# Kernel tuning notes

Measured on AMD Instinct MI355X. Metric: run time of the kernel, lower is better.

The kernel has to match this reference:

```python
import jax, jax.numpy as jnp
import numpy as np

B, S, DIM = 1, 2048, 2048
HEADS, KV_HEADS = 32, 8
DH = DIM // HEADS          # 64 head dim
G = HEADS // KV_HEADS      # 4 grouped queries per kv head
CBLK = 16                  # compress block size (stride == block size)
SBLK = 16                  # selection (fine) block size
NSEL = 8                   # top-k selected blocks
WIN = 64                   # sliding window size
SCALE = DH ** -0.5
NEG = -1e30
CDIM = CBLK * DH


def setup_inputs():
    key = jax.random.key(0)
    ks = jax.random.split(key, 16)
    def rnd(i, shape, sc=0.02):
        return jax.random.normal(ks[i], shape, dtype=jnp.float32) * sc
    dim_inner, dim_kv = HEADS * DH, KV_HEADS * DH
    return {
        "hidden_states": jax.random.normal(ks[0], (B, S, DIM), dtype=jnp.float32),
        "w_qkv": rnd(1, (DIM, dim_inner + 2 * dim_kv)),
        "k_pos": rnd(2, (KV_HEADS, CBLK, DH)),
        "v_pos": rnd(3, (KV_HEADS, CBLK, DH)),
        "k_cw1": rnd(4, (CDIM, CDIM)), "k_cb1": jnp.zeros((CDIM,), jnp.float32),
        "k_cw2": rnd(5, (CDIM, DH)),  "k_cb2": jnp.zeros((DH,), jnp.float32),
        "v_cw1": rnd(6, (CDIM, CDIM)), "v_cb1": jnp.zeros((CDIM,), jnp.float32),
        "v_cw2": rnd(7, (CDIM, DH)),  "v_cb2": jnp.zeros((DH,), jnp.float32),
        "mem_ck": rnd(8, (KV_HEADS, 1, DH)),
        "mem_cv": rnd(9, (KV_HEADS, 1, DH)),
        "w_gate": rnd(10, (DIM, 3 * HEADS)),
        "b_gate": jnp.tile(jnp.array([-2.0, -2.0, 2.0], jnp.float32), HEADS),
        "w_out": rnd(11, (dim_inner, DIM)),
    }


def _rope(x, pos):
    # rotary-embedding-torch style: interleaved pairs (x0,x1),(x2,x3),...
    d = x.shape[-1]
    inv = 1.0 / (10000.0 ** (jnp.arange(0, d, 2, dtype=jnp.float32) / d))
    ang = pos[:, None] * inv[None, :]
    cos, sin = jnp.cos(ang), jnp.sin(ang)
    x1, x2 = x[..., 0::2], x[..., 1::2]
    return jnp.stack([x1 * cos - x2 * sin, x1 * sin + x2 * cos], axis=-1).reshape(x.shape)


def _forward(x, w_qkv, k_pos, v_pos, k_cw1, k_cb1, k_cw2, k_cb2,
             v_cw1, v_cb1, v_cw2, v_cb2, mem_ck, mem_cv, w_gate, b_gate, w_out):
    b, n, _ = x.shape
    di, dkv = HEADS * DH, KV_HEADS * DH
    qkv = x @ w_qkv
    # head index = kv_head * G + grouped_query, matching 'b n (h d) -> b h n d'
    q = qkv[..., :di].reshape(b, n, KV_HEADS, G, DH).transpose(0, 2, 3, 1, 4)    # [b,kh,g,n,d]
    k = qkv[..., di:di + dkv].reshape(b, n, KV_HEADS, DH).transpose(0, 2, 1, 3)  # [b,kh,n,d]
    v = qkv[..., di + dkv:].reshape(b, n, KV_HEADS, DH).transpose(0, 2, 1, 3)

    # ---- branch 1: compressed-block attention (pre-rotary q/k, intra-block abs pos) ----
    nc = n // CBLK
    kb = k[:, :, :nc * CBLK].reshape(b, KV_HEADS, nc, CBLK, DH) + k_pos[None, :, None]
    vb = v[:, :, :nc * CBLK].reshape(b, KV_HEADS, nc, CBLK, DH) + v_pos[None, :, None]
    ck = jax.nn.relu(kb.reshape(b, KV_HEADS, nc, CDIM) @ k_cw1 + k_cb1) @ k_cw2 + k_cb2
    cv = jax.nn.relu(vb.reshape(b, KV_HEADS, nc, CDIM) @ v_cw1 + v_cb1) @ v_cw2 + v_cb2
    ck = jnp.concatenate([jnp.broadcast_to(mem_ck[None], (b, KV_HEADS, 1, DH)), ck], axis=2)
    cv = jnp.concatenate([jnp.broadcast_to(mem_cv[None], (b, KV_HEADS, 1, DH)), cv], axis=2)
    csim = jnp.einsum('bhgnd,bhjd->bhgnj', q, ck) * SCALE
    ck_last = jnp.concatenate([jnp.array([-1]), (jnp.arange(nc) + 1) * CBLK - 1])
    cmask = ck_last[None, :] < jnp.arange(n)[:, None]                            # [n, 1+nc]
    csim = jnp.where(cmask, csim, NEG)
    c_out = jnp.einsum('bhgnj,bhjd->bhgnd', jax.nn.softmax(csim, -1), cv)

    # ---- importance scores -> top-k selected blocks (shared across grouped queries) ----
    imp = csim[..., 1:].mean(axis=2)                                             # [b,kh,n,nc]
    imp = jnp.concatenate([jnp.full(imp.shape[:-1] + (1,), -1e3, imp.dtype), imp], axis=-1)
    imp = jax.nn.softmax(imp, -1)[..., 1:]
    sel_vals, sel_idx = jax.lax.top_k(imp, NSEL)                                 # [b,kh,n,NSEL]
    fine_gate_mask = sel_vals > 1e-10

    # rotary for fine + sliding branches
    pos = jnp.arange(n, dtype=jnp.float32)
    rq, rk = _rope(q, pos), _rope(k, pos)

    # ---- branch 2: fine attention over top-k selected blocks + causal own block ----
    nf = n // SBLK
    own = jnp.broadcast_to((jnp.arange(n) // SBLK)[None, None, :, None], (b, KV_HEADS, n, 1))
    idx = jnp.concatenate([sel_idx, own], axis=-1)                               # [b,kh,n,NSEL+1]
    kblocks = rk.reshape(b, KV_HEADS, nf, SBLK, DH)
    vblocks = v.reshape(b, KV_HEADS, nf, SBLK, DH)
    bi = jnp.arange(b)[:, None, None, None]
    hi = jnp.arange(KV_HEADS)[None, :, None, None]
    fk = kblocks[bi, hi, idx].reshape(b, KV_HEADS, n, (NSEL + 1) * SBLK, DH)
    fv = vblocks[bi, hi, idx].reshape(b, KV_HEADS, n, (NSEL + 1) * SBLK, DH)
    sel_m = jnp.repeat(fine_gate_mask[..., None], SBLK, -1).reshape(b, KV_HEADS, n, NSEL * SBLK)
    diag_m = (jnp.arange(n) % SBLK)[:, None] >= jnp.arange(SBLK)[None, :]        # own-block causal
    fmask = jnp.concatenate(
        [sel_m, jnp.broadcast_to(diag_m[None, None], (b, KV_HEADS, n, SBLK))], axis=-1)
    fsim = jnp.einsum('bhgnd,bhnjd->bhgnj', rq, fk) * SCALE
    fsim = jnp.where(fmask[:, :, None], fsim, NEG)
    f_out = jnp.einsum('bhgnj,bhnjd->bhgnd', jax.nn.softmax(fsim, -1), fv)

    # ---- branch 3: sliding-window attention (current + previous window, exact size) ----
    nwin = n // WIN
    qw = rq.reshape(b, KV_HEADS, G, nwin, WIN, DH)
    kw = rk.reshape(b, KV_HEADS, nwin, WIN, DH)
    vw = v.reshape(b, KV_HEADS, nwin, WIN, DH)
    kcat = jnp.concatenate([jnp.concatenate([jnp.zeros_like(kw[:, :, :1]), kw[:, :, :-1]], 2), kw], 3)
    vcat = jnp.concatenate([jnp.concatenate([jnp.zeros_like(vw[:, :, :1]), vw[:, :, :-1]], 2), vw], 3)
    ssim = jnp.einsum('bhgwid,bhwjd->bhgwij', qw, kcat) * SCALE
    i_, j_ = jnp.arange(WIN), jnp.arange(2 * WIN)
    delta = i_[:, None] - (j_[None, :] - WIN)                                    # query - key distance
    smask = ((delta >= 0) & (delta <= WIN))[None] \
        & ((jnp.arange(nwin) > 0)[:, None, None] | (j_ >= WIN)[None, None, :])
    ssim = jnp.where(smask[None, None, None], ssim, NEG)
    s_out = jnp.einsum('bhgwij,bhwjd->bhgwid', jax.nn.softmax(ssim, -1), vcat)
    s_out = s_out.reshape(b, KV_HEADS, G, n, DH)

    # ---- learned sigmoid gate combine (compressed, fine, sliding) + out proj ----
    gates = jax.nn.sigmoid(x @ w_gate + b_gate).reshape(b, n, KV_HEADS, G, 3).transpose(0, 2, 3, 1, 4)
    out = gates[..., 0:1] * c_out + gates[..., 1:2] * f_out + gates[..., 2:3] * s_out
    out = out.transpose(0, 3, 1, 2, 4).reshape(b, n, HEADS * DH)
    return out @ w_out


def reference(hidden_states, w_qkv, k_pos, v_pos, k_cw1, k_cb1, k_cw2, k_cb2,
              v_cw1, v_cb1, v_cw2, v_cb2, mem_ck, mem_cv, w_gate, b_gate, w_out):
    return _forward(hidden_states, w_qkv, k_pos, v_pos, k_cw1, k_cb1, k_cw2, k_cb2,
                    v_cw1, v_cb1, v_cw2, v_cb2, mem_ck, mem_cv, w_gate, b_gate, w_out)
```

## Files before the change

### kernel.cpp

```cpp
#include <hip/hip_runtime.h>
#include <hip/hip_bf16.h>
#include <math.h>

using bf16 = __hip_bfloat16;
typedef __attribute__((ext_vector_type(8))) short short8;
typedef __attribute__((ext_vector_type(4))) float f32x4;

#define SCALE 0.125f
#define NEGV  -1e30f
#define QS    3200

__device__ __forceinline__ float bf2f(bf16 x) { return __bfloat162float(x); }
__device__ __forceinline__ bf16  f2bf(float x) { return __float2bfloat16(x); }
__device__ __forceinline__ short f2bs(float x) {
  bf16 b = __float2bfloat16(x);
  return *reinterpret_cast<short*>(&b);
}
__device__ __forceinline__ float dot4(float4 a, float4 b) {
  return a.x * b.x + a.y * b.y + a.z * b.z + a.w * b.w;
}
__device__ __forceinline__ float sigm(float x) { return 1.0f / (1.0f + __expf(-x)); }

__device__ __forceinline__ void wavefence() {
  asm volatile("s_waitcnt lgkmcnt(0)" ::: "memory");
// ... 232 lines not shown
{
  int idx = blockIdx.x * 256 + threadIdx.x;
  if (idx >= 8 * 160 * 64) return;
  int h = idx / (160 * 64), r = (idx >> 6) % 160, d = idx & 63;
  if (r >= 129) { cvT[((size_t)h * 64 + d) * 160 + r] = f2bf(0.f); return; }
  float kv, vv;
  if (r == 0) {
    kv = bf2f(mem_ck[h * 64 + d]);
    vv = bf2f(mem_cv[h * 64 + d]);
  } else {
    kv = ckpre[((size_t)h * 128 + r - 1) * 64 + d] + bf2f(k_cb2[d]);
    vv = cvpre[((size_t)h * 128 + r - 1) * 64 + d] + bf2f(v_cb2[d]);
  }
  ck[((size_t)h * 129 + r) * 64 + d] = kv;
  cvT[((size_t)h * 64 + d) * 160 + r] = f2bf(vv);
}

__global__ __launch_bounds__(256, 4)
void compress_attn_kernel(const float* __restrict__ qkv, const float* __restrict__ ck,
                          const bf16* __restrict__ cvT,
                          float* __restrict__ outpre, int* __restrict__ sel)
{
  __shared__ __align__(16) char un[4][5632];
  const int tid = threadIdx.x, w = tid >> 6, lane = tid & 63;
  const int quad = lane >> 4, l16 = lane & 15;
  const int h = blockIdx.x >> 7;
  const int jv = blockIdx.x & 127;
  const int i0 = jv * 16 + w * 4;
  float* qs = (float*)un[w];
  bf16*  ps = (bf16*)un[w];

  #pragma unroll
  for (int m = 0; m < 16; m++)
    qs[m * 64 + lane] = qkv[(size_t)(i0 + (m >> 2)) * QS + (h * 4 + (m & 3)) * 64 + lane];
  wavefence();

  const float* kh = ck + (size_t)h * 129 * 64;
  const float4* k0 = (const float4*)(kh + lane * 64);
  const float4* k1 = (const float4*)(kh + (lane + 64) * 64);
  const bool two = (jv >= 64);

  float d0[4][4], d1[4][4];
  #pragma unroll
  for (int T = 0; T < 4; T++)
    #pragma unroll
    for (int g = 0; g < 4; g++) { d0[T][g] = 0.f; d1[T][g] = 0.f; }

  if (two) {
    #pragma unroll 4
    for (int t = 0; t < 16; t++) {
      float4 a = k0[t], b = k1[t];
      #pragma unroll
      for (int T = 0; T < 4; T++)
        #pragma unroll
        for (int g = 0; g < 4; g++) {
          float4 qv = *(const float4*)&qs[(T * 4 + g) * 64 + t * 4];
          d0[T][g] += dot4(qv, a);
          d1[T][g] += dot4(qv, b);
        }
    }
  } else {
    #pragma unroll 4
    for (int t = 0; t < 16; t++) {
      float4 a = k0[t];
      #pragma unroll
      for (int T = 0; T < 4; T++)
        #pragma unroll
        for (int g = 0; g < 4; g++) {
          float4 qv = *(const float4*)&qs[(T * 4 + g) * 64 + t * 4];
          d0[T][g] += dot4(qv, a);
        }
    }
  }
  wavefence();

  const bool v0 = (lane == 0) || (lane <= jv);
  const bool v1 = two && (lane + 64 <= jv);
  float imp0[4], imp1[4];
  #pragma unroll
  for (int T = 0; T < 4; T++) {
    #pragma unroll
    for (int g = 0; g < 4; g++) {
      d0[T][g] = v0 ? d0[T][g] * SCALE : NEGV;
      d1[T][g] = v1 ? d1[T][g] * SCALE : NEGV;
    }
    imp0[T] = (d0[T][0] + d0[T][1] + d0[T][2] + d0[T][3]) * 0.25f;
    imp1[T] = (d1[T][0] + d1[T][1] + d1[T][2] + d1[T][3]) * 0.25f;
  }

  float mx[4][4], sm[4][4];
  #pragma unroll
  for (int T = 0; T < 4; T++)
    #pragma unroll
    for (int g = 0; g < 4; g++) mx[T][g] = fmaxf(d0[T][g], d1[T][g]);
  #pragma unroll
  for (int off = 32; off; off >>= 1)
    #pragma unroll
    for (int T = 0; T < 4; T++)
      #pragma unroll
      for (int g = 0; g < 4; g++) mx[T][g] = fmaxf(mx[T][g], __shfl_xor(mx[T][g], off));
  #pragma unroll
  for (int T = 0; T < 4; T++)
    #pragma unroll
    for (int g = 0; g < 4; g++) {
      d0[T][g] = __expf(d0[T][g] - mx[T][g]);
      d1[T][g] = __expf(d1[T][g] - mx[T][g]);
      sm[T][g] = d0[T][g] + d1[T][g];
    }
  #pragma unroll
  for (int off = 32; off; off >>= 1)
    #pragma unroll
    for (int T = 0; T < 4; T++)
      #pragma unroll
      for (int g = 0; g < 4; g++) sm[T][g] += __shfl_xor(sm[T][g], off);
  #pragma unroll
  for (int T = 0; T < 4; T++)
    #pragma unroll
    for (int g = 0; g < 4; g++) {
      float inv = 1.0f / sm[T][g];
      ps[(T * 4 + g) * 176 + lane] = f2bf(d0[T][g] * inv);
      if (two) ps[(T * 4 + g) * 176 + 64 + lane] = f2bf(d1[T][g] * inv);
    }

  float q0[4], q1[4];
  {
    float mxi[4], smi[4], e0[4], e1[4];
    #pragma unroll
    for (int T = 0; T < 4; T++) {
      float iv0 = (lane == 0) ? -1000.0f : imp0[T];
      mxi[T] = fmaxf(iv0, imp1[T]);
      q0[T] = iv0;
      q1[T] = imp1[T];
    }
    #pragma unroll
    for (int off = 32; off; off >>= 1)
      #pragma unroll
      for (int T = 0; T < 4; T++) mxi[T] = fmaxf(mxi[T], __shfl_xor(mxi[T], off));
    #pragma unroll
    for (int T = 0; T < 4; T++) {
      e0[T] = __expf(q0[T] - mxi[T]);
      e1[T] = __expf(q1[T] - mxi[T]);
      smi[T] = e0[T] + e1[T];
    }
    #pragma unroll
    for (int off = 32; off; off >>= 1)
      #pragma unroll
      for (int T = 0; T < 4; T++) smi[T] += __shfl_xor(smi[T], off);
    #pragma unroll
    for (int T = 0; T < 4; T++) {
      float inv = 1.0f / smi[T];
      q0[T] = (lane >= 1) ? e0[T] * inv : -1.0f;
      q1[T] = e1[T] * inv;
    }
  }
  for (int s = 0; s < 8; s++) {
    float bv[4]; int bj[4];
    #pragma unroll
    for (int T = 0; T < 4; T++) {
      bv[T] = q0[T]; bj[T] = lane;
      if (q1[T] > bv[T]) { bv[T] = q1[T]; bj[T] = lane + 64; }
    }
    #pragma unroll
    for (int off = 32; off; off >>= 1)
      #pragma unroll
      for (int T = 0; T < 4; T++) {
        float ov = __shfl_xor(bv[T], off); int oj = __shfl_xor(bj[T], off);
        if (ov > bv[T] || (ov == bv[T] && oj < bj[T])) { bv[T] = ov; bj[T] = oj; }
      }
    #pragma unroll
    for (int T = 0; T < 4; T++) {
      if (lane == 0)
        sel[((size_t)h * 2048 + i0 + T) * 8 + s] = (bv[T] > 1e-10f) ? (bj[T] - 1) : -1;
      if (bj[T] == lane)           q0[T] = -1.0f;
      else if (bj[T] == lane + 64) q1[T] = -1.0f;
    }
  }

  const int iq = i0 + quad;
  float g0v[4];
  #pragma unroll
  for (int g = 0; g < 4; g++)
    g0v[g] = sigm(qkv[(size_t)iq * QS + 3072 + (h * 4 + g) * 3 + 0]);
  wavefence();

  const bf16* cvh = cvT + (size_t)h * 64 * 160;
  const int nks = (jv >> 5) + 1;
  f32x4 acc[4];
  #pragma unroll
  for (int dt = 0; dt < 4; dt++) acc[dt] = f32x4{0, 0, 0, 0};
  for (int ks = 0; ks < nks; ks++) {
    short8 ap = *(const short8*)(const void*)&ps[l16 * 176 + ks * 32 + quad * 8];
    #pragma unroll
    for (int dt = 0; dt < 4; dt++) {
      const bf16* cp = cvh + (size_t)(dt * 16 + l16) * 160 + ks * 32 + quad * 8;
      short8 bv = *(const short8*)(const void*)cp;
      acc[dt] = __builtin_amdgcn_mfma_f32_16x16x32_bf16(ap, bv, acc[dt], 0, 0, 0);
    }
  }

  #pragma unroll
  for (int g = 0; g < 4; g++) {
    const int hq = h * 4 + g;
    #pragma unroll
    for (int dt = 0; dt < 4; dt++)
      outpre[(size_t)iq * 2048 + hq * 64 + dt * 16 + l16] = g0v[g] * acc[dt][g];
  }
}

__global__ __launch_bounds__(256)
void rope_kernel(const float* __restrict__ qkv, bf16* __restrict__ qb,
                 bf16* __restrict__ kb)
{
  int idx = blockIdx.x * 256 + threadIdx.x;
  if (idx >= 2048 * 40 * 32) return;
  int m = idx & 31, hh = (idx >> 5) % 40, i = idx / 1280;
  int col = (hh < 32) ? hh * 64 + 2 * m : 2048 + (hh - 32) * 64 + 2 * m;
  const float* p = qkv + (size_t)i * QS + col;
  float x1 = p[0], x2 = p[1];
  float inv = exp2f(-0.41524101186092029f * (float)m);
  float ang = (float)i * inv;
  float s, c;
  __sincosf(ang, &s, &c);
  float r1 = x1 * c - x2 * s;
  float r2 = x1 * s + x2 * c;
  unsigned pack = ((unsigned)(unsigned short)f2bs(r1)) |
                  (((unsigned)(unsigned short)f2bs(r2)) << 16);
  if (hh < 32) {
    int h = hh >> 2, g = hh & 3;
    *(unsigned*)&qb[(((size_t)h * 2048 + i) * 4 + g) * 64 + 2 * m] = pack;
  } else {
    *(unsigned*)&kb[((size_t)(hh - 32) * 2048 + i) * 64 + 2 * m] = pack;
  }
}

__global__ __launch_bounds__(256)
void slide_attn_kernel(const float* __restrict__ qkv, const bf16* __restrict__ qb,
                       const bf16* __restrict__ kb, const bf16* __restrict__ vt,
                       bf16* __restrict__ oslide)
{
  __shared__ __align__(16) bf16 ps[4][16][104];
  const int tid = threadIdx.x, w = tid >> 6, lane = tid & 63;
  const int quad = lane >> 4, l16 = lane & 15;
  const int h = blockIdx.x >> 7, i0 = (blockIdx.x & 127) << 4;
  const int g = w;

  const bf16* qp = qb + (((size_t)h * 2048 + i0 + l16) * 4 + g) * 64 + quad * 8;
  short8 aq0 = *(const short8*)(const void*)qp;
  short8 aq1 = *(const short8*)(const void*)(qp + 32);

  const bf16* kbh = kb + (size_t)h * 2048 * 64;
  const int jbase = i0 - 64;

  f32x4 cs[5];
  #pragma unroll
  for (int t = 0; t < 5; t++) {
    int jr = jbase + t * 16 + l16;
    int jc = jr < 0 ? 0 : jr;
    const bf16* kp = kbh + (size_t)jc * 64 + quad * 8;
    short8 b0 = *(const short8*)(const void*)kp;
    short8 b1 = *(const short8*)(const void*)(kp + 32);
    f32x4 c = {0.f, 0.f, 0.f, 0.f};
    c = __builtin_amdgcn_mfma_f32_16x16x32_bf16(aq0, b0, c, 0, 0, 0);
    c = __builtin_amdgcn_mfma_f32_16x16x32_bf16(aq1, b1, c, 0, 0, 0);
    cs[t] = c;
  }

  float pr[5][4];
  #pragma unroll
  for (int r = 0; r < 4; r++) {
    int ti = i0 + quad * 4 + r;
    float mx = -3.0e38f;
    #pragma unroll
    for (int t = 0; t < 5; t++) {
      int j = jbase + t * 16 + l16;
      bool valid = (j >= 0) && (j >= ti - 64) && (j <= ti);
      float sv = valid ? cs[t][r] * SCALE : -3.0e38f;
      pr[t][r] = sv;
      mx = fmaxf(mx, sv);
    }
    #pragma unroll
    for (int off = 8; off; off >>= 1) mx = fmaxf(mx, __shfl_xor(mx, off));
    float sm = 0.f;
    #pragma unroll
    for (int t = 0; t < 5; t++) { float e = __expf(pr[t][r] - mx); pr[t][r] = e; sm += e; }
    #pragma unroll
    for (int off = 8; off; off >>= 1) sm += __shfl_xor(sm, off);
    float inv = 1.0f / sm;
    #pragma unroll
    for (int t = 0; t < 5; t++) pr[t][r] *= inv;
  }

  #pragma unroll
  for (int t = 0; t < 5; t++)
    #pragma unroll
    for (int r = 0; r < 4; r++)
      ps[w][quad * 4 + r][t * 16 + l16] = f2bf(pr[t][r]);
  #pragma unroll
  for (int r = 0; r < 4; r++) ps[w][l16][80 + quad * 4 + r] = f2bf(0.f);
  wavefence();

  const bf16* vth = vt + (size_t)h * 64 * 2176 + 64;
  f32x4 os[4];
  #pragma unroll
  for (int dt = 0; dt < 4; dt++) os[dt] = f32x4{0,0,0,0};
  #pragma unroll
  for (int ks = 0; ks < 3; ks++) {
    short8 ap = *(const short8*)(const void*)&ps[w][l16][ks * 32 + quad * 8];
    int coff = jbase + ks * 32 + quad * 8;
    #pragma unroll
    for (int dt = 0; dt < 4; dt++) {
      const bf16* vp = vth + (size_t)(dt * 16 + l16) * 2176 + coff;
      short8 bv = *(const short8*)(const void*)vp;
      os[dt] = __builtin_amdgcn_mfma_f32_16x16x32_bf16(ap, bv, os[dt], 0, 0, 0);
    }
  }

  #pragma unroll
  for (int r = 0; r < 4; r++) {
    int ti = i0 + quad * 4 + r;
    int hq = h * 4 + g;
    float g2 = sigm(qkv[(size_t)ti * QS + 3072 + hq * 3 + 2]);
    #pragma unroll
    for (int dt = 0; dt < 4; dt++)
      oslide[(size_t)ti * 2048 + hq * 64 + dt * 16 + l16] = f2bf(g2 * os[dt][r]);
  }
}

__global__ __launch_bounds__(256)
void fine_attn_kernel(const float* __restrict__ qkv, const int* __restrict__ sel,
                      const float* __restrict__ outpre, const bf16* __restrict__ oslide,
                      const bf16* __restrict__ qb, const bf16* __restrict__ kb,
                      const bf16* __restrict__ vt, bf16* __restrict__ outpre_b)
{
  __shared__ __align__(16) bf16 psf[4][16][176];
  const int tid = threadIdx.x, w = tid >> 6, lane = tid & 63;
  const int quad = lane >> 4, l16 = lane & 15;
  const int h = blockIdx.x >> 7;
  const int i0 = (blockIdx.x & 127) * 16 + w * 4;

  const bf16* qp = qb + (((size_t)h * 2048 + i0 + (l16 >> 2)) * 4 + (l16 & 3)) * 64 + quad * 8;
  short8 aq0 = *(const short8*)(const void*)qp;
  short8 aq1 = *(const short8*)(const void*)(qp + 32);

  const bf16* kbh = kb + (size_t)h * 2048 * 64;
  const int own = i0 >> 4;
  const int selbase = (h * 2048 + i0) * 8;

  f32x4 ct[9];

  {
    const bf16* kp = kbh + (size_t)(own * 16 + l16) * 64 + quad * 8;
    short8 b0 = *(const short8*)(const void*)kp;
    short8 b1 = *(const short8*)(const void*)(kp + 32);
    f32x4 c = {0.f, 0.f, 0.f, 0.f};
    c = __builtin_amdgcn_mfma_f32_16x16x32_bf16(aq0, b0, c, 0, 0, 0);
    c = __builtin_amdgcn_mfma_f32_16x16x32_bf16(aq1, b1, c, 0, 0, 0);
    const int imod = (i0 + quad) & 15;
    #pragma unroll
    for (int g = 0; g < 4; g++)
      ct[8][g] = (l16 <= imod) ? c[g] * SCALE : -3.0e38f;
  }

  int vb[4][8];
  #pragma unroll
  for (int T = 0; T < 4; T++) {
    #pragma unroll
    for (int t = 0; t < 8; t++) {
      int blk = __builtin_amdgcn_readfirstlane(sel[selbase + T * 8 + t]);
      bool tv = (blk >= 0);
      int blc = tv ? blk : 0;
      vb[T][t] = blc;
      const bf16* kp = kbh + (size_t)(blc * 16 + l16) * 64 + quad * 8;
      short8 b0 = *(const short8*)(const void*)kp;
      short8 b1 = *(const short8*)(const void*)(kp + 32);
      f32x4 c = {0.f, 0.f, 0.f, 0.f};
      c = __builtin_amdgcn_mfma_f32_16x16x32_bf16(aq0, b0, c, 0, 0, 0);
      c = __builtin_amdgcn_mfma_f32_16x16x32_bf16(aq1, b1, c, 0, 0, 0);
      #pragma unroll
      for (int g = 0; g < 4; g++) {
        float v = tv ? c[g] * SCALE : -3.0e38f;
        if (T == 0) ct[t][g] = v;
        else if (quad == T) ct[t][g] = v;
      }
    }
  }

  float fm[4], fsum[4];
  #pragma unroll
  for (int g = 0; g < 4; g++) fm[g] = -3.0e38f;
  #pragma unroll
  for (int t = 0; t < 9; t++)
    #pragma unroll
    for (int g = 0; g < 4; g++) fm[g] = fmaxf(fm[g], ct[t][g]);
  #pragma unroll
  for (int g = 0; g < 4; g++) {
    #pragma unroll
    for (int off = 8; off; off >>= 1) fm[g] = fmaxf(fm[g], __shfl_xor(fm[g], off));
    fsum[g] = 0.f;
  }
  #pragma unroll
  for (int t = 0; t < 9; t++)
    #pragma unroll
    for (int g = 0; g < 4; g++) {
      float e = __expf(ct[t][g] - fm[g]);
      ct[t][g] = e;
      fsum[g] += e;
    }
  #pragma unroll
  for (int g = 0; g < 4; g++) {
    #pragma unroll
    for (int off = 8; off; off >>= 1) fsum[g] += __shfl_xor(fsum[g], off);
    fsum[g] = 1.0f / fsum[g];
  }

  #pragma unroll
  for (int t = 0; t < 9; t++)
    #pragma unroll
    for (int g = 0; g < 4; g++)
      psf[w][quad * 4 + g][t * 16 + l16] = f2bf(ct[t][g] * fsum[g]);
  #pragma unroll
  for (int g = 0; g < 4; g++)
    psf[w][quad * 4 + g][144 + l16] = f2bf(0.f);

  const int iq = i0 + quad;
  float g1v[4], prev[4][4];
  #pragma unroll
  for (int g = 0; g < 4; g++) {
    const int hq = h * 4 + g;
    g1v[g] = sigm(qkv[(size_t)iq * QS + 3072 + hq * 3 + 1]);
    #pragma unroll
    for (int dt = 0; dt < 4; dt++) {
      size_t oidx = (size_t)iq * 2048 + hq * 64 + dt * 16 + l16;
      prev[g][dt] = outpre[oidx] + bf2f(oslide[oidx]);
    }
  }
  wavefence();

  const bf16* vth = vt + (size_t)h * 64 * 2176 + 64;

  f32x4 obase[4];
  {
    short8 ap = *(const short8*)(const void*)&psf[w][l16][128 + quad * 8];
    int coff = (((quad >> 1) == 0) ? own : 0) * 16 + (quad & 1) * 8;
    #pragma unroll
    for (int dt = 0; dt < 4; dt++) {
      const bf16* vp = vth + (size_t)(dt * 16 + l16) * 2176 + coff;
      short8 bv = *(const short8*)(const void*)vp;
      f32x4 z = {0.f, 0.f, 0.f, 0.f};
      obase[dt] = __builtin_amdgcn_mfma_f32_16x16x32_bf16(ap, bv, z, 0, 0, 0);
    }
  }

  f32x4 osave[4];
  #pragma unroll
  for (int T = 0; T < 4; T++) {
    f32x4 acc[4];
    #pragma unroll
    for (int dt = 0; dt < 4; dt++) acc[dt] = obase[dt];
    #pragma unroll
    for (int ks = 0; ks < 4; ks++) {
      short8 ap = *(const short8*)(const void*)&psf[w][l16][ks * 32 + quad * 8];
      int blkv = ((quad >> 1) == 0) ? vb[T][ks * 2] : vb[T][ks * 2 + 1];
      int coff = blkv * 16 + (quad & 1) * 8;
      #pragma unroll
      for (int dt = 0; dt < 4; dt++) {
        const bf16* vp = vth + (size_t)(dt * 16 + l16) * 2176 + coff;
        short8 bv = *(const short8*)(const void*)vp;
        acc[dt] = __builtin_amdgcn_mfma_f32_16x16x32_bf16(ap, bv, acc[dt], 0, 0, 0);
      }
    }
    #pragma unroll
    for (int dt = 0; dt < 4; dt++) {
      if (T == 0) osave[dt] = acc[dt];
      else if (quad == T) osave[dt] = acc[dt];
    }
  }

  #pragma unroll
  for (int g = 0; g < 4; g++) {
    const int hq = h * 4 + g;
    #pragma unroll
    for (int dt = 0; dt < 4; dt++) {
      size_t oidx = (size_t)iq * 2048 + hq * 64 + dt * 16 + l16;
      outpre_b[oidx] = f2bf(prev[g][dt] + g1v[g] * osave[dt][g]);
    }
  }
}

extern "C" void kernel_launch(void* const* d_in, const int* in_sizes, int n_in,
                              void* d_out, int out_size, void* d_ws, size_t ws_size,
                              hipStream_t stream)
{
  char* ws = (char*)d_ws;
  size_t off = 0;
  auto alloc = [&](size_t bytes) -> char* {
    char* p = ws + off; off = (off + bytes + 255) & ~(size_t)255; return p;
  };

  int* flag = (int*)alloc(256);
  bf16* inb[17];
  for (int i = 0; i < 17; i++) {
    if (i == 1 || i == 4 || i == 8 || i == 14 || i == 16) { inb[i] = nullptr; continue; }
    inb[i] = (bf16*)alloc((size_t)in_sizes[i] * sizeof(bf16));
  }
  bf16* w_qkvT = (bf16*)alloc(3200ull * 2048 * 2);
  bf16* k_cw1T = (bf16*)alloc(1024ull * 1024 * 2);
  bf16* v_cw1T = (bf16*)alloc(1024ull * 1024 * 2);
  bf16* w_outT = (bf16*)alloc(2048ull * 2048 * 2);

  float* qkv      = (float*)alloc(2048ull * QS * 4);
  float* outpre   = (float*)alloc(2048ull * 2048 * 4);
  bf16*  kvb      = (bf16*)alloc(2048ull * 1024 * 2);
  bf16*  hid      = (bf16*)alloc(2048ull * 1024 * 2);
  float* ckcvpre  = (float*)alloc(2048ull * 64 * 4);
  float* ckb      = (float*)alloc(8ull * 129 * 64 * 4);
  int*   sel      = (int*)alloc(8ull * 2048 * 8 * 4);
  bf16*  qbuf     = (bf16*)alloc(8ull * 2048 * 4 * 64 * 2);
  bf16*  kbuf     = (bf16*)alloc(8ull * 2048 * 64 * 2);
  bf16*  vtb      = (bf16*)alloc(8ull * 64 * 2176 * 2);
  bf16*  outpre_b = kvb;
  bf16*  cvT      = k_cw1T;
  bf16*  oslide   = (bf16*)w_qkvT;

  const bf16 *xb = inb[0], *k_posb = inb[2], *v_posb = inb[3],
             *k_cb1b = inb[5], *k_cw2b = inb[6], *k_cb2b = inb[7],
             *v_cb1b = inb[9], *v_cw2b = inb[10], *v_cb2b = inb[11],
             *mem_ckb = inb[12], *mem_cvb = inb[13], *b_gateb = inb[15];

  detect_mode_kernel<<<1, 64, 0, stream>>>(d_in[15], flag);

  ConvArgs ca;
  int total = 0, nseg = 0;
  for (int i = 0; i < 17; i++) {
    if (i == 1 || i == 4 || i == 8 || i == 14 || i == 16) continue;
    ca.src[nseg] = d_in[i];
    ca.dst[nseg] = inb[i];
    ca.start[nseg] = total;
// ... 12 lines not shown
  hipMemsetAsync(vtb, 0, 8ull * 64 * 2176 * 2, stream);

  gemm_bt_kernel<0,0,0,1,0><<<dim3(25, 16), 256, 0, stream>>>(
      xb, w_qkvT, nullptr, nullptr, b_gateb, qkv, 2048, QS, 2048, 0, nullptr);

  rope_kernel<<<10240, 256, 0, stream>>>(qkv, qbuf, kbuf);
  vtrans_kernel<<<dim3(32, 8), 256, 0, stream>>>(qkv, vtb);

  prep_kb_kernel<<<4096, 256, 0, stream>>>(qkv, k_posb, v_posb, kvb, kvb + 1024 * 1024);
  gemm_bt_kernel<1,1,1,0,0><<<dim3(8, 16), 256, 0, stream>>>(
      kvb, k_cw1T, v_cw1T, k_cb1b, v_cb1b, hid, 2048, 1024, 1024, 1024, nullptr);
  gemm64_splitk_kernel<<<dim3(1, 32, 4), 256, 0, stream>>>(
      hid, k_cw2b, v_cw2b, ckcvpre, 2048, 64, 1024, 1024, 256);
  concat_kernel<<<320, 256, 0, stream>>>(ckcvpre, ckcvpre + 1024 * 64,
                                         mem_ckb, mem_cvb, k_cb2b, v_cb2b, ckb, cvT);
  compress_attn_kernel<<<1024, 256, 0, stream>>>(qkv, ckb, cvT, outpre, sel);
  slide_attn_kernel<<<1024, 256, 0, stream>>>(qkv, qbuf, kbuf, vtb, oslide);
  fine_attn_kernel<<<1024, 256, 0, stream>>>(qkv, sel, outpre, oslide, qbuf, kbuf, vtb, outpre_b);
  gemm_bt_kernel<0,0,0,0,1><<<dim3(16, 16), 256, 0, stream>>>(
      outpre_b, w_outT, nullptr, nullptr, nullptr, d_out, 2048, 2048, 2048, 0, flag);
}
```

Measured before the change: 499.6 us.

## Fuse compressed, sliding and fine attention into one kernel

Merges the compressed-attention, sliding-window and fine-selection kernels into a single kernel. Each wave now computes all three branch outputs for its queries, keeps the top-k selection in registers, and writes the gated combination once. This removes the intermediate fp32 outpre, oslide and sel buffers, their global round trips, and two launches. The cost is higher register and LDS pressure per block, which may reduce occupancy. The sliding-window tile mapping is also changed to match the fine kernel's 4-query-by-4-group layout.

```diff
diff --git a/kernel.cpp b/kernel.cpp
--- a/kernel.cpp
+++ b/kernel.cpp
@@ -270,197 +270,6 @@
   }
   ck[((size_t)h * 129 + r) * 64 + d] = kv;
   cvT[((size_t)h * 64 + d) * 160 + r] = f2bf(vv);
-}
-
-__global__ __launch_bounds__(256, 4)
-void compress_attn_kernel(const float* __restrict__ qkv, const float* __restrict__ ck,
-                          const bf16* __restrict__ cvT,
-                          float* __restrict__ outpre, int* __restrict__ sel)
-{
-  __shared__ __align__(16) char un[4][5632];
-  const int tid = threadIdx.x, w = tid >> 6, lane = tid & 63;
-  const int quad = lane >> 4, l16 = lane & 15;
-  const int h = blockIdx.x >> 7;
-  const int jv = blockIdx.x & 127;
-  const int i0 = jv * 16 + w * 4;
-  float* qs = (float*)un[w];
-  bf16*  ps = (bf16*)un[w];
-
-  #pragma unroll
-  for (int m = 0; m < 16; m++)
-    qs[m * 64 + lane] = qkv[(size_t)(i0 + (m >> 2)) * QS + (h * 4 + (m & 3)) * 64 + lane];
-  wavefence();
-
-  const float* kh = ck + (size_t)h * 129 * 64;
-  const float4* k0 = (const float4*)(kh + lane * 64);
-  const float4* k1 = (const float4*)(kh + (lane + 64) * 64);
-  const bool two = (jv >= 64);
-
-  float d0[4][4], d1[4][4];
-  #pragma unroll
-  for (int T = 0; T < 4; T++)
-    #pragma unroll
-    for (int g = 0; g < 4; g++) { d0[T][g] = 0.f; d1[T][g] = 0.f; }
-
-  if (two) {
-    #pragma unroll 4
-    for (int t = 0; t < 16; t++) {
-      float4 a = k0[t], b = k1[t];
-      #pragma unroll
-      for (int T = 0; T < 4; T++)
-        #pragma unroll
-        for (int g = 0; g < 4; g++) {
-          float4 qv = *(const float4*)&qs[(T * 4 + g) * 64 + t * 4];
-          d0[T][g] += dot4(qv, a);
-          d1[T][g] += dot4(qv, b);
-        }
-    }
-  } else {
-    #pragma unroll 4
-    for (int t = 0; t < 16; t++) {
-      float4 a = k0[t];
-      #pragma unroll
-      for (int T = 0; T < 4; T++)
-        #pragma unroll
-        for (int g = 0; g < 4; g++) {
-          float4 qv = *(const float4*)&qs[(T * 4 + g) * 64 + t * 4];
-          d0[T][g] += dot4(qv, a);
-        }
-    }
-  }
-  wavefence();
-
-  const bool v0 = (lane == 0) || (lane <= jv);
-  const bool v1 = two && (lane + 64 <= jv);
-  float imp0[4], imp1[4];
-  #pragma unroll
-  for (int T = 0; T < 4; T++) {
-    #pragma unroll
-    for (int g = 0; g < 4; g++) {
-      d0[T][g] = v0 ? d0[T][g] * SCALE : NEGV;
-      d1[T][g] = v1 ? d1[T][g] * SCALE : NEGV;
-    }
-    imp0[T] = (d0[T][0] + d0[T][1] + d0[T][2] + d0[T][3]) * 0.25f;
-    imp1[T] = (d1[T][0] + d1[T][1] + d1[T][2] + d1[T][3]) * 0.25f;
-  }
-
-  float mx[4][4], sm[4][4];
-  #pragma unroll
-  for (int T = 0; T < 4; T++)
-    #pragma unroll
-    for (int g = 0; g < 4; g++) mx[T][g] = fmaxf(d0[T][g], d1[T][g]);
-  #pragma unroll
-  for (int off = 32; off; off >>= 1)
-    #pragma unroll
-    for (int T = 0; T < 4; T++)
-      #pragma unroll
-      for (int g = 0; g < 4; g++) mx[T][g] = fmaxf(mx[T][g], __shfl_xor(mx[T][g], off));
-  #pragma unroll
-  for (int T = 0; T < 4; T++)
-    #pragma unroll
-    for (int g = 0; g < 4; g++) {
-      d0[T][g] = __expf(d0[T][g] - mx[T][g]);
-      d1[T][g] = __expf(d1[T][g] - mx[T][g]);
-      sm[T][g] = d0[T][g] + d1[T][g];
-    }
-  #pragma unroll
-  for (int off = 32; off; off >>= 1)
-    #pragma unroll
-    for (int T = 0; T < 4; T++)
-      #pragma unroll
-      for (int g = 0; g < 4; g++) sm[T][g] += __shfl_xor(sm[T][g], off);
-  #pragma unroll
-  for (int T = 0; T < 4; T++)
-    #pragma unroll
-    for (int g = 0; g < 4; g++) {
-      float inv = 1.0f / sm[T][g];
-      ps[(T * 4 + g) * 176 + lane] = f2bf(d0[T][g] * inv);
-      if (two) ps[(T * 4 + g) * 176 + 64 + lane] = f2bf(d1[T][g] * inv);
-    }
-
-  float q0[4], q1[4];
-  {
-    float mxi[4], smi[4], e0[4], e1[4];
-    #pragma unroll
-    for (int T = 0; T < 4; T++) {
-      float iv0 = (lane == 0) ? -1000.0f : imp0[T];
-      mxi[T] = fmaxf(iv0, imp1[T]);
-      q0[T] = iv0;
-      q1[T] = imp1[T];
-    }
-    #pragma unroll
-    for (int off = 32; off; off >>= 1)
-      #pragma unroll
-      for (int T = 0; T < 4; T++) mxi[T] = fmaxf(mxi[T], __shfl_xor(mxi[T], off));
-    #pragma unroll
-    for (int T = 0; T < 4; T++) {
-      e0[T] = __expf(q0[T] - mxi[T]);
-      e1[T] = __expf(q1[T] - mxi[T]);
-      smi[T] = e0[T] + e1[T];
-    }
-    #pragma unroll
-    for (int off = 32; off; off >>= 1)
-      #pragma unroll
-      for (int T = 0; T < 4; T++) smi[T] += __shfl_xor(smi[T], off);
-    #pragma unroll
-    for (int T = 0; T < 4; T++) {
-      float inv = 1.0f / smi[T];
-      q0[T] = (lane >= 1) ? e0[T] * inv : -1.0f;
-      q1[T] = e1[T] * inv;
-    }
-  }
-  for (int s = 0; s < 8; s++) {
-    float bv[4]; int bj[4];
-    #pragma unroll
-    for (int T = 0; T < 4; T++) {
-      bv[T] = q0[T]; bj[T] = lane;
-      if (q1[T] > bv[T]) { bv[T] = q1[T]; bj[T] = lane + 64; }
-    }
-    #pragma unroll
-    for (int off = 32; off; off >>= 1)
-      #pragma unroll
-      for (int T = 0; T < 4; T++) {
-        float ov = __shfl_xor(bv[T], off); int oj = __shfl_xor(bj[T], off);
-        if (ov > bv[T] || (ov == bv[T] && oj < bj[T])) { bv[T] = ov; bj[T] = oj; }
-      }
-    #pragma unroll
-    for (int T = 0; T < 4; T++) {
-      if (lane == 0)
-        sel[((size_t)h * 2048 + i0 + T) * 8 + s] = (bv[T] > 1e-10f) ? (bj[T] - 1) : -1;
-      if (bj[T] == lane)           q0[T] = -1.0f;
-      else if (bj[T] == lane + 64) q1[T] = -1.0f;
-    }
-  }
-
-  const int iq = i0 + quad;
-  float g0v[4];
-  #pragma unroll
-  for (int g = 0; g < 4; g++)
-    g0v[g] = sigm(qkv[(size_t)iq * QS + 3072 + (h * 4 + g) * 3 + 0]);
-  wavefence();
-
-  const bf16* cvh = cvT + (size_t)h * 64 * 160;
-  const int nks = (jv >> 5) + 1;
-  f32x4 acc[4];
-  #pragma unroll
-  for (int dt = 0; dt < 4; dt++) acc[dt] = f32x4{0, 0, 0, 0};
-  for (int ks = 0; ks < nks; ks++) {
-    short8 ap = *(const short8*)(const void*)&ps[l16 * 176 + ks * 32 + quad * 8];
-    #pragma unroll
-    for (int dt = 0; dt < 4; dt++) {
-      const bf16* cp = cvh + (size_t)(dt * 16 + l16) * 160 + ks * 32 + quad * 8;
-      short8 bv = *(const short8*)(const void*)cp;
-      acc[dt] = __builtin_amdgcn_mfma_f32_16x16x32_bf16(ap, bv, acc[dt], 0, 0, 0);
-    }
-  }
-
-  #pragma unroll
-  for (int g = 0; g < 4; g++) {
-    const int hq = h * 4 + g;
-    #pragma unroll
-    for (int dt = 0; dt < 4; dt++)
-      outpre[(size_t)iq * 2048 + hq * 64 + dt * 16 + l16] = g0v[g] * acc[dt][g];
-  }
 }
 
 __global__ __launch_bounds__(256)
@@ -490,142 +299,226 @@
 }
 
 __global__ __launch_bounds__(256)
-void slide_attn_kernel(const float* __restrict__ qkv, const bf16* __restrict__ qb,
+void attn_fused_kernel(const float* __restrict__ qkv, const float* __restrict__ ck,
+                       const bf16* __restrict__ cvT, const bf16* __restrict__ qb,
                        const bf16* __restrict__ kb, const bf16* __restrict__ vt,
-                       bf16* __restrict__ oslide)
-{
-  __shared__ __align__(16) bf16 ps[4][16][104];
+                       bf16* __restrict__ outb)
+{
+  __shared__ __align__(16) char un[4][5632];
+  __shared__ __align__(16) bf16 ss[4][16][104];
   const int tid = threadIdx.x, w = tid >> 6, lane = tid & 63;
   const int quad = lane >> 4, l16 = lane & 15;
-  const int h = blockIdx.x >> 7, i0 = (blockIdx.x & 127) << 4;
-  const int g = w;
-
-  const bf16* qp = qb + (((size_t)h * 2048 + i0 + l16) * 4 + g) * 64 + quad * 8;
+  const int h = blockIdx.x >> 7;
+  const int jv = blockIdx.x & 127;
+  const int i0 = jv * 16 + w * 4;
+  float* qs = (float*)un[w];
+  bf16*  pc = (bf16*)un[w];
+
+  const bf16* qp = qb + (((size_t)h * 2048 + i0 + (l16 >> 2)) * 4 + (l16 & 3)) * 64 + quad * 8;
   short8 aq0 = *(const short8*)(const void*)qp;
   short8 aq1 = *(const short8*)(const void*)(qp + 32);
 
   const bf16* kbh = kb + (size_t)h * 2048 * 64;
-  const int jbase = i0 - 64;
-
-  f32x4 cs[5];
+  const int ti = i0 + quad;
+
+  const int ib = i0 - 64, r0 = ib & 7, jb8 = ib - r0;
+  f32x4 cw[5];
   #pragma unroll
   for (int t = 0; t < 5; t++) {
-    int jr = jbase + t * 16 + l16;
-    int jc = jr < 0 ? 0 : jr;
+    int jr = jb8 + t * 16 + l16;
+    int jc = jr < 0 ? 0 : (jr > 2047 ? 2047 : jr);
     const bf16* kp = kbh + (size_t)jc * 64 + quad * 8;
     short8 b0 = *(const short8*)(const void*)kp;
     short8 b1 = *(const short8*)(const void*)(kp + 32);
     f32x4 c = {0.f, 0.f, 0.f, 0.f};
     c = __builtin_amdgcn_mfma_f32_16x16x32_bf16(aq0, b0, c, 0, 0, 0);
     c = __builtin_amdgcn_mfma_f32_16x16x32_bf16(aq1, b1, c, 0, 0, 0);
-    cs[t] = c;
-  }
-
-  float pr[5][4];
-  #pragma unroll
-  for (int r = 0; r < 4; r++) {
-    int ti = i0 + quad * 4 + r;
-    float mx = -3.0e38f;
-    #pragma unroll
-    for (int t = 0; t < 5; t++) {
-      int j = jbase + t * 16 + l16;
-      bool valid = (j >= 0) && (j >= ti - 64) && (j <= ti);
-      float sv = valid ? cs[t][r] * SCALE : -3.0e38f;
-      pr[t][r] = sv;
-      mx = fmaxf(mx, sv);
-    }
-    #pragma unroll
-    for (int off = 8; off; off >>= 1) mx = fmaxf(mx, __shfl_xor(mx, off));
-    float sm = 0.f;
-    #pragma unroll
-    for (int t = 0; t < 5; t++) { float e = __expf(pr[t][r] - mx); pr[t][r] = e; sm += e; }
-    #pragma unroll
-    for (int off = 8; off; off >>= 1) sm += __shfl_xor(sm, off);
-    float inv = 1.0f / sm;
-    #pragma unroll
-    for (int t = 0; t < 5; t++) pr[t][r] *= inv;
-  }
-
-  #pragma unroll
-  for (int t = 0; t < 5; t++)
-    #pragma unroll
-    for (int r = 0; r < 4; r++)
-      ps[w][quad * 4 + r][t * 16 + l16] = f2bf(pr[t][r]);
-  #pragma unroll
-  for (int r = 0; r < 4; r++) ps[w][l16][80 + quad * 4 + r] = f2bf(0.f);
-  wavefence();
-
-  const bf16* vth = vt + (size_t)h * 64 * 2176 + 64;
-  f32x4 os[4];
-  #pragma unroll
-  for (int dt = 0; dt < 4; dt++) os[dt] = f32x4{0,0,0,0};
-  #pragma unroll
-  for (int ks = 0; ks < 3; ks++) {
-    short8 ap = *(const short8*)(const void*)&ps[w][l16][ks * 32 + quad * 8];
-    int coff = jbase + ks * 32 + quad * 8;
-    #pragma unroll
-    for (int dt = 0; dt < 4; dt++) {
-      const bf16* vp = vth + (size_t)(dt * 16 + l16) * 2176 + coff;
-      short8 bv = *(const short8*)(const void*)vp;
-      os[dt] = __builtin_amdgcn_mfma_f32_16x16x32_bf16(ap, bv, os[dt], 0, 0, 0);
-    }
-  }
-
-  #pragma unroll
-  for (int r = 0; r < 4; r++) {
-    int ti = i0 + quad * 4 + r;
-    int hq = h * 4 + g;
-    float g2 = sigm(qkv[(size_t)ti * QS + 3072 + hq * 3 + 2]);
-    #pragma unroll
-    for (int dt = 0; dt < 4; dt++)
-      oslide[(size_t)ti * 2048 + hq * 64 + dt * 16 + l16] = f2bf(g2 * os[dt][r]);
-  }
-}
-
-__global__ __launch_bounds__(256)
-void fine_attn_kernel(const float* __restrict__ qkv, const int* __restrict__ sel,
-                      const float* __restrict__ outpre, const bf16* __restrict__ oslide,
-                      const bf16* __restrict__ qb, const bf16* __restrict__ kb,
-                      const bf16* __restrict__ vt, bf16* __restrict__ outpre_b)
-{
-  __shared__ __align__(16) bf16 psf[4][16][176];
-  const int tid = threadIdx.x, w = tid >> 6, lane = tid & 63;
-  const int quad = lane >> 4, l16 = lane & 15;
-  const int h = blockIdx.x >> 7;
-  const int i0 = (blockIdx.x & 127) * 16 + w * 4;
-
-  const bf16* qp = qb + (((size_t)h * 2048 + i0 + (l16 >> 2)) * 4 + (l16 & 3)) * 64 + quad * 8;
-  short8 aq0 = *(const short8*)(const void*)qp;
-  short8 aq1 = *(const short8*)(const void*)(qp + 32);
-
-  const bf16* kbh = kb + (size_t)h * 2048 * 64;
-  const int own = i0 >> 4;
-  const int selbase = (h * 2048 + i0) * 8;
+    bool valid = (jr >= 0) && (jr >= ti - 64) && (jr <= ti);
+    #pragma unroll
+    for (int g = 0; g < 4; g++) cw[t][g] = valid ? c[g] * SCALE : -3.0e38f;
+  }
 
   f32x4 ct[9];
-
   {
-    const bf16* kp = kbh + (size_t)(own * 16 + l16) * 64 + quad * 8;
+    const bf16* kp = kbh + (size_t)(jv * 16 + l16) * 64 + quad * 8;
     short8 b0 = *(const short8*)(const void*)kp;
     short8 b1 = *(const short8*)(const void*)(kp + 32);
     f32x4 c = {0.f, 0.f, 0.f, 0.f};
     c = __builtin_amdgcn_mfma_f32_16x16x32_bf16(aq0, b0, c, 0, 0, 0);
     c = __builtin_amdgcn_mfma_f32_16x16x32_bf16(aq1, b1, c, 0, 0, 0);
-    const int imod = (i0 + quad) & 15;
+    const int imod = w * 4 + quad;
     #pragma unroll
     for (int g = 0; g < 4; g++)
       ct[8][g] = (l16 <= imod) ? c[g] * SCALE : -3.0e38f;
   }
 
-  int vb[4][8];
+  #pragma unroll
+  for (int m = 0; m < 16; m++)
+    qs[m * 64 + lane] = qkv[(size_t)(i0 + (m >> 2)) * QS + (h * 4 + (m & 3)) * 64 + lane];
+  wavefence();
+
+  const float* kh = ck + (size_t)h * 129 * 64;
+  const float4* k0 = (const float4*)(kh + lane * 64);
+  const float4* k1 = (const float4*)(kh + (lane + 64) * 64);
+  const bool two = (jv >= 64);
+
+  float d0[4][4], d1[4][4];
+  #pragma unroll
+  for (int T = 0; T < 4; T++)
+    #pragma unroll
+    for (int g = 0; g < 4; g++) { d0[T][g] = 0.f; d1[T][g] = 0.f; }
+
+  if (two) {
+    #pragma unroll 4
+    for (int t = 0; t < 16; t++) {
+      float4 a = k0[t], b = k1[t];
+      #pragma unroll
+      for (int T = 0; T < 4; T++)
+        #pragma unroll
+        for (int g = 0; g < 4; g++) {
+          float4 qv = *(const float4*)&qs[(T * 4 + g) * 64 + t * 4];
+          d0[T][g] += dot4(qv, a);
+          d1[T][g] += dot4(qv, b);
+        }
+    }
+  } else {
+    #pragma unroll 4
+    for (int t = 0; t < 16; t++) {
+      float4 a = k0[t];
+      #pragma unroll
+      for (int T = 0; T < 4; T++)
+        #pragma unroll
+        for (int g = 0; g < 4; g++) {
+          float4 qv = *(const float4*)&qs[(T * 4 + g) * 64 + t * 4];
+          d0[T][g] += dot4(qv, a);
+        }
+    }
+  }
+  wavefence();
+
+  const bool v0 = (lane == 0) || (lane <= jv);
+  const bool v1 = two && (lane + 64 <= jv);
+  float imp0[4], imp1[4];
   #pragma unroll
   for (int T = 0; T < 4; T++) {
     #pragma unroll
+    for (int g = 0; g < 4; g++) {
+      d0[T][g] = v0 ? d0[T][g] * SCALE : NEGV;
+      d1[T][g] = v1 ? d1[T][g] * SCALE : NEGV;
+    }
+    imp0[T] = (d0[T][0] + d0[T][1] + d0[T][2] + d0[T][3]) * 0.25f;
+    imp1[T] = (d1[T][0] + d1[T][1] + d1[T][2] + d1[T][3]) * 0.25f;
+  }
+
+  {
+    float mx[4][4], sm[4][4];
+    #pragma unroll
+    for (int T = 0; T < 4; T++)
+      #pragma unroll
+      for (int g = 0; g < 4; g++) mx[T][g] = fmaxf(d0[T][g], d1[T][g]);
+    #pragma unroll
+    for (int off = 32; off; off >>= 1)
+      #pragma unroll
+      for (int T = 0; T < 4; T++)
+        #pragma unroll
+        for (int g = 0; g < 4; g++) mx[T][g] = fmaxf(mx[T][g], __shfl_xor(mx[T][g], off));
+    #pragma unroll
+    for (int T = 0; T < 4; T++)
+      #pragma unroll
+      for (int g = 0; g < 4; g++) {
+        d0[T][g] = __expf(d0[T][g] - mx[T][g]);
+        d1[T][g] = __expf(d1[T][g] - mx[T][g]);
+        sm[T][g] = d0[T][g] + d1[T][g];
+      }
+    #pragma unroll
+    for (int off = 32; off; off >>= 1)
+      #pragma unroll
+      for (int T = 0; T < 4; T++)
+        #pragma unroll
+        for (int g = 0; g < 4; g++) sm[T][g] += __shfl_xor(sm[T][g], off);
+    #pragma unroll
+    for (int T = 0; T < 4; T++)
+      #pragma unroll
+      for (int g = 0; g < 4; g++) {
+        float inv = 1.0f / sm[T][g];
+        pc[(T * 4 + g) * 176 + lane] = f2bf(d0[T][g] * inv);
+        if (two) pc[(T * 4 + g) * 176 + 64 + lane] = f2bf(d1[T][g] * inv);
+      }
+  }
+
+  int vbsel[4][8];
+  {
+    float q0[4], q1[4];
+    float mxi[4], smi[4], e0[4], e1[4];
+    #pragma unroll
+    for (int T = 0; T < 4; T++) {
+      float iv0 = (lane == 0) ? -1000.0f : imp0[T];
+      mxi[T] = fmaxf(iv0, imp1[T]);
+      q0[T] = iv0;
+      q1[T] = imp1[T];
+    }
+    #pragma unroll
+    for (int off = 32; off; off >>= 1)
+      #pragma unroll
+      for (int T = 0; T < 4; T++) mxi[T] = fmaxf(mxi[T], __shfl_xor(mxi[T], off));
+    #pragma unroll
+    for (int T = 0; T < 4; T++) {
+      e0[T] = __expf(q0[T] - mxi[T]);
+      e1[T] = __expf(q1[T] - mxi[T]);
+      smi[T] = e0[T] + e1[T];
+    }
+    #pragma unroll
+    for (int off = 32; off; off >>= 1)
+      #pragma unroll
+      for (int T = 0; T < 4; T++) smi[T] += __shfl_xor(smi[T], off);
+    #pragma unroll
+    for (int T = 0; T < 4; T++) {
+      float inv = 1.0f / smi[T];
+      q0[T] = (lane >= 1) ? e0[T] * inv : -1.0f;
+      q1[T] = e1[T] * inv;
+    }
+    #pragma unroll
+    for (int s = 0; s < 8; s++) {
+      float bv[4]; int bj[4];
+      #pragma unroll
+      for (int T = 0; T < 4; T++) {
+        bv[T] = q0[T]; bj[T] = lane;
+        if (q1[T] > bv[T]) { bv[T] = q1[T]; bj[T] = lane + 64; }
+      }
+      #pragma unroll
+      for (int off = 32; off; off >>= 1)
+        #pragma unroll
+        for (int T = 0; T < 4; T++) {
+          float ov = __shfl_xor(bv[T], off); int oj = __shfl_xor(bj[T], off);
+          if (ov > bv[T] || (ov == bv[T] && oj < bj[T])) { bv[T] = ov; bj[T] = oj; }
+        }
+      #pragma unroll
+      for (int T = 0; T < 4; T++) {
+        vbsel[T][s] = (bv[T] > 1e-10f) ? (bj[T] - 1) : -1;
+        if (bj[T] == lane)           q0[T] = -1.0f;
+        else if (bj[T] == lane + 64) q1[T] = -1.0f;
+      }
+    }
+  }
+
+  float g0v[4], g1v[4], g2v[4];
+  #pragma unroll
+  for (int g = 0; g < 4; g++) {
+    const int hq = h * 4 + g;
+    g0v[g] = sigm(qkv[(size_t)ti * QS + 3072 + hq * 3 + 0]);
+    g1v[g] = sigm(qkv[(size_t)ti * QS + 3072 + hq * 3 + 1]);
+    g2v[g] = sigm(qkv[(size_t)ti * QS + 3072 + hq * 3 + 2]);
+  }
+
+  int vbc[4][8];
+  #pragma unroll
+  for (int T = 0; T < 4; T++) {
+    #pragma unroll
     for (int t = 0; t < 8; t++) {
-      int blk = __builtin_amdgcn_readfirstlane(sel[selbase + T * 8 + t]);
+      int blk = __builtin_amdgcn_readfirstlane(vbsel[T][t]);
       bool tv = (blk >= 0);
       int blc = tv ? blk : 0;
-      vb[T][t] = blc;
+      vbc[T][t] = blc;
       const bf16* kp = kbh + (size_t)(blc * 16 + l16) * 64 + quad * 8;
       short8 b0 = *(const short8*)(const void*)kp;
       short8 b1 = *(const short8*)(const void*)(kp + 32);
@@ -640,64 +533,128 @@
       }
     }
   }
-
-  float fm[4], fsum[4];
-  #pragma unroll
-  for (int g = 0; g < 4; g++) fm[g] = -3.0e38f;
+  wavefence();
+
+  const bf16* cvh = cvT + (size_t)h * 64 * 160;
+  const int nks = (jv >> 5) + 1;
+  f32x4 oc[4];
+  #pragma unroll
+  for (int dt = 0; dt < 4; dt++) oc[dt] = f32x4{0, 0, 0, 0};
+  for (int ks = 0; ks < nks; ks++) {
+    short8 ap = *(const short8*)(const void*)&pc[l16 * 176 + ks * 32 + quad * 8];
+    #pragma unroll
+    for (int dt = 0; dt < 4; dt++) {
+      const bf16* cp = cvh + (size_t)(dt * 16 + l16) * 160 + ks * 32 + quad * 8;
+      short8 bv = *(const short8*)(const void*)cp;
+      oc[dt] = __builtin_amdgcn_mfma_f32_16x16x32_bf16(ap, bv, oc[dt], 0, 0, 0);
+    }
+  }
+
+  float fsum[4];
+  {
+    float fm[4];
+    #pragma unroll
+    for (int g = 0; g < 4; g++) fm[g] = -3.0e38f;
+    #pragma unroll
+    for (int t = 0; t < 9; t++)
+      #pragma unroll
+      for (int g = 0; g < 4; g++) fm[g] = fmaxf(fm[g], ct[t][g]);
+    #pragma unroll
+    for (int g = 0; g < 4; g++) {
+      #pragma unroll
+      for (int off = 8; off; off >>= 1) fm[g] = fmaxf(fm[g], __shfl_xor(fm[g], off));
+      fsum[g] = 0.f;
+    }
+    #pragma unroll
+    for (int t = 0; t < 9; t++)
+      #pragma unroll
+      for (int g = 0; g < 4; g++) {
+        float e = __expf(ct[t][g] - fm[g]);
+        ct[t][g] = e;
+        fsum[g] += e;
+      }
+    #pragma unroll
+    for (int g = 0; g < 4; g++) {
+      #pragma unroll
+      for (int off = 8; off; off >>= 1) fsum[g] += __shfl_xor(fsum[g], off);
+      fsum[g] = 1.0f / fsum[g];
+    }
+  }
+
+  {
+    float sm_[4], ssum[4];
+    #pragma unroll
+    for (int g = 0; g < 4; g++) sm_[g] = -3.0e38f;
+    #pragma unroll
+    for (int t = 0; t < 5; t++)
+      #pragma unroll
+      for (int g = 0; g < 4; g++) sm_[g] = fmaxf(sm_[g], cw[t][g]);
+    #pragma unroll
+    for (int g = 0; g < 4; g++) {
+      #pragma unroll
+      for (int off = 8; off; off >>= 1) sm_[g] = fmaxf(sm_[g], __shfl_xor(sm_[g], off));
+      ssum[g] = 0.f;
+    }
+    #pragma unroll
+    for (int t = 0; t < 5; t++)
+      #pragma unroll
+      for (int g = 0; g < 4; g++) {
+        float e = __expf(cw[t][g] - sm_[g]);
+        cw[t][g] = e;
+        ssum[g] += e;
+      }
+    #pragma unroll
+    for (int g = 0; g < 4; g++) {
+      #pragma unroll
+      for (int off = 8; off; off >>= 1) ssum[g] += __shfl_xor(ssum[g], off);
+      ssum[g] = 1.0f / ssum[g];
+    }
+    #pragma unroll
+    for (int t = 0; t < 5; t++)
+      #pragma unroll
+      for (int g = 0; g < 4; g++) cw[t][g] *= ssum[g];
+  }
+  wavefence();
+
   #pragma unroll
   for (int t = 0; t < 9; t++)
     #pragma unroll
-    for (int g = 0; g < 4; g++) fm[g] = fmaxf(fm[g], ct[t][g]);
-  #pragma unroll
-  for (int g = 0; g < 4; g++) {
-    #pragma unroll
-    for (int off = 8; off; off >>= 1) fm[g] = fmaxf(fm[g], __shfl_xor(fm[g], off));
-    fsum[g] = 0.f;
-  }
-  #pragma unroll
-  for (int t = 0; t < 9; t++)
-    #pragma unroll
-    for (int g = 0; g < 4; g++) {
-      float e = __expf(ct[t][g] - fm[g]);
-      ct[t][g] = e;
-      fsum[g] += e;
-    }
-  #pragma unroll
-  for (int g = 0; g < 4; g++) {
-    #pragma unroll
-    for (int off = 8; off; off >>= 1) fsum[g] += __shfl_xor(fsum[g], off);
-    fsum[g] = 1.0f / fsum[g];
-  }
-
-  #pragma unroll
-  for (int t = 0; t < 9; t++)
-    #pragma unroll
     for (int g = 0; g < 4; g++)
-      psf[w][quad * 4 + g][t * 16 + l16] = f2bf(ct[t][g] * fsum[g]);
+      pc[(quad * 4 + g) * 176 + t * 16 + l16] = f2bf(ct[t][g] * fsum[g]);
   #pragma unroll
   for (int g = 0; g < 4; g++)
-    psf[w][quad * 4 + g][144 + l16] = f2bf(0.f);
-
-  const int iq = i0 + quad;
-  float g1v[4], prev[4][4];
-  #pragma unroll
-  for (int g = 0; g < 4; g++) {
-    const int hq = h * 4 + g;
-    g1v[g] = sigm(qkv[(size_t)iq * QS + 3072 + hq * 3 + 1]);
+    pc[(quad * 4 + g) * 176 + 144 + l16] = f2bf(0.f);
+  #pragma unroll
+  for (int t = 0; t < 5; t++)
+    #pragma unroll
+    for (int g = 0; g < 4; g++)
+      ss[w][quad * 4 + g][t * 16 + l16] = f2bf(cw[t][g]);
+  #pragma unroll
+  for (int r = 0; r < 4; r++)
+    ss[w][quad * 4 + r][80 + l16] = f2bf(0.f);
+  wavefence();
+
+  const bf16* vth = vt + (size_t)h * 64 * 2176 + 64;
+
+  f32x4 os[4];
+  #pragma unroll
+  for (int dt = 0; dt < 4; dt++) os[dt] = f32x4{0, 0, 0, 0};
+  #pragma unroll
+  for (int ks = 0; ks < 3; ks++) {
+    short8 ap = *(const short8*)(const void*)&ss[w][l16][ks * 32 + quad * 8];
+    int coff = jb8 + ks * 32 + quad * 8;
     #pragma unroll
     for (int dt = 0; dt < 4; dt++) {
-      size_t oidx = (size_t)iq * 2048 + hq * 64 + dt * 16 + l16;
-      prev[g][dt] = outpre[oidx] + bf2f(oslide[oidx]);
-    }
-  }
-  wavefence();
-
-  const bf16* vth = vt + (size_t)h * 64 * 2176 + 64;
+      const bf16* vp = vth + (size_t)(dt * 16 + l16) * 2176 + coff;
+      short8 bv = *(const short8*)(const void*)vp;
+      os[dt] = __builtin_amdgcn_mfma_f32_16x16x32_bf16(ap, bv, os[dt], 0, 0, 0);
+    }
+  }
 
   f32x4 obase[4];
   {
-    short8 ap = *(const short8*)(const void*)&psf[w][l16][128 + quad * 8];
-    int coff = (((quad >> 1) == 0) ? own : 0) * 16 + (quad & 1) * 8;
+    short8 ap = *(const short8*)(const void*)&pc[l16 * 176 + 128 + quad * 8];
+    int coff = (((quad >> 1) == 0) ? jv : 0) * 16 + (quad & 1) * 8;
     #pragma unroll
     for (int dt = 0; dt < 4; dt++) {
       const bf16* vp = vth + (size_t)(dt * 16 + l16) * 2176 + coff;
@@ -706,8 +663,7 @@
       obase[dt] = __builtin_amdgcn_mfma_f32_16x16x32_bf16(ap, bv, z, 0, 0, 0);
     }
   }
-
-  f32x4 osave[4];
+  f32x4 of[4];
   #pragma unroll
   for (int T = 0; T < 4; T++) {
     f32x4 acc[4];
@@ -715,8 +671,8 @@
     for (int dt = 0; dt < 4; dt++) acc[dt] = obase[dt];
     #pragma unroll
     for (int ks = 0; ks < 4; ks++) {
-      short8 ap = *(const short8*)(const void*)&psf[w][l16][ks * 32 + quad * 8];
-      int blkv = ((quad >> 1) == 0) ? vb[T][ks * 2] : vb[T][ks * 2 + 1];
+      short8 ap = *(const short8*)(const void*)&pc[l16 * 176 + ks * 32 + quad * 8];
+      int blkv = ((quad >> 1) == 0) ? vbc[T][ks * 2] : vbc[T][ks * 2 + 1];
       int coff = blkv * 16 + (quad & 1) * 8;
       #pragma unroll
       for (int dt = 0; dt < 4; dt++) {
@@ -727,8 +683,8 @@
     }
     #pragma unroll
     for (int dt = 0; dt < 4; dt++) {
-      if (T == 0) osave[dt] = acc[dt];
-      else if (quad == T) osave[dt] = acc[dt];
+      if (T == 0) of[dt] = acc[dt];
+      else if (quad == T) of[dt] = acc[dt];
     }
   }
 
@@ -737,8 +693,8 @@
     const int hq = h * 4 + g;
     #pragma unroll
     for (int dt = 0; dt < 4; dt++) {
-      size_t oidx = (size_t)iq * 2048 + hq * 64 + dt * 16 + l16;
-      outpre_b[oidx] = f2bf(prev[g][dt] + g1v[g] * osave[dt][g]);
+      size_t oidx = (size_t)ti * 2048 + hq * 64 + dt * 16 + l16;
+      outb[oidx] = f2bf(g0v[g] * oc[dt][g] + g1v[g] * of[dt][g] + g2v[g] * os[dt][g]);
     }
   }
 }
@@ -765,18 +721,15 @@
   bf16* w_outT = (bf16*)alloc(2048ull * 2048 * 2);
 
   float* qkv      = (float*)alloc(2048ull * QS * 4);
-  float* outpre   = (float*)alloc(2048ull * 2048 * 4);
   bf16*  kvb      = (bf16*)alloc(2048ull * 1024 * 2);
   bf16*  hid      = (bf16*)alloc(2048ull * 1024 * 2);
   float* ckcvpre  = (float*)alloc(2048ull * 64 * 4);
   float* ckb      = (float*)alloc(8ull * 129 * 64 * 4);
-  int*   sel      = (int*)alloc(8ull * 2048 * 8 * 4);
   bf16*  qbuf     = (bf16*)alloc(8ull * 2048 * 4 * 64 * 2);
   bf16*  kbuf     = (bf16*)alloc(8ull * 2048 * 64 * 2);
   bf16*  vtb      = (bf16*)alloc(8ull * 64 * 2176 * 2);
   bf16*  outpre_b = kvb;
   bf16*  cvT      = k_cw1T;
-  bf16*  oslide   = (bf16*)w_qkvT;
 
   const bf16 *xb = inb[0], *k_posb = inb[2], *v_posb = inb[3],
              *k_cb1b = inb[5], *k_cw2b = inb[6], *k_cb2b = inb[7],
@@ -819,9 +772,9 @@
       hid, k_cw2b, v_cw2b, ckcvpre, 2048, 64, 1024, 1024, 256);
   concat_kernel<<<320, 256, 0, stream>>>(ckcvpre, ckcvpre + 1024 * 64,
                                          mem_ckb, mem_cvb, k_cb2b, v_cb2b, ckb, cvT);
-  compress_attn_kernel<<<1024, 256, 0, stream>>>(qkv, ckb, cvT, outpre, sel);
-  slide_attn_kernel<<<1024, 256, 0, stream>>>(qkv, qbuf, kbuf, vtb, oslide);
-  fine_attn_kernel<<<1024, 256, 0, stream>>>(qkv, sel, outpre, oslide, qbuf, kbuf, vtb, outpre_b);
+
+  attn_fused_kernel<<<1024, 256, 0, stream>>>(qkv, ckb, cvT, qbuf, kbuf, vtb, outpre_b);
+
   gemm_bt_kernel<0,0,0,0,1><<<dim3(16, 16), 256, 0, stream>>>(
       outpre_b, w_outT, nullptr, nullptr, nullptr, d_out, 2048, 2048, 2048, 0, flag);
 }
```

Result: slower. 556.5 us (+11.4%).
